# Kernel tuning notes

Hardware: AMD Instinct MI355X
Metric: run time of the kernel (lower is better)

The kernel has to match this reference:

```python
import jax, jax.numpy as jnp
import numpy as np

LATENT, H, A, L, BOS = 256, 512, 64, 128, 0


def setup_inputs() -> dict:
    key = jax.random.key(0)
    ks = jax.random.split(key, 20)
    s = 0.05
    return {
        "latent": jax.random.normal(ks[0], (4096, LATENT), jnp.float32),
        "target": jax.random.normal(ks[1], (4096, L, A), jnp.float32),
        # latent dense decoder: Linear(LATENT,H), Tanh, Linear(H,H), Tanh, Linear(H,H)
        "Wd1": jax.random.normal(ks[2], (H, LATENT), jnp.float32) * s,
        "bd1": jnp.zeros((H,), jnp.float32),
        "Wd2": jax.random.normal(ks[3], (H, H), jnp.float32) * s,
        "bd2": jnp.zeros((H,), jnp.float32),
        "Wd3": jax.random.normal(ks[4], (H, H), jnp.float32) * s,
        "bd3": jnp.zeros((H,), jnp.float32),
        # GRU (torch layout: W_ih [3H,A], W_hh [3H,H], gate order r,z,n)
        "W_ih": jax.random.normal(ks[5], (3 * H, A), jnp.float32) * s,
        "W_hh": jax.random.normal(ks[6], (3 * H, H), jnp.float32) * s,
        "b_ih": jnp.zeros((3 * H,), jnp.float32),
        "b_hh": jnp.zeros((3 * H,), jnp.float32),
        # per-step dense decoder: Linear(H,H), Tanh, Linear(H,A), Tanh, Linear(A,A)
        "Wm1": jax.random.normal(ks[7], (H, H), jnp.float32) * s,
        "bm1": jnp.zeros((H,), jnp.float32),
        "Wm2": jax.random.normal(ks[8], (A, H), jnp.float32) * s,
        "bm2": jnp.zeros((A,), jnp.float32),
        "Wm3": jax.random.normal(ks[9], (A, A), jnp.float32) * s,
        "bm3": jnp.zeros((A,), jnp.float32),
    }


def reference(latent, target, Wd1, bd1, Wd2, bd2, Wd3, bd3,
              W_ih, W_hh, b_ih, b_hh, Wm1, bm1, Wm2, bm2, Wm3, bm3):
    B = latent.shape[0]
    # initial hidden from latent: Linear-Tanh-Linear-Tanh-Linear
    h = jnp.tanh(latent @ Wd1.T + bd1)
    h = jnp.tanh(h @ Wd2.T + bd2)
    h = h @ Wd3.T + bd3  # [B, H]

    # BOS pseudo one-hot: -16 everywhere, +16 at BOS index
    bos = jnp.full((B, A), -16.0, jnp.float32).at[:, BOS].set(16.0)

    # teacher forcing: step i (1..L-1) consumes [bos, target[:,1], ..., target[:,L-2]]
    xs = jnp.concatenate([bos[None], jnp.swapaxes(target[:, 1:L - 1], 0, 1)], axis=0)  # [L-1, B, A]

    def step(h, x):
        gi = x @ W_ih.T + b_ih  # [B, 3H]
        gh = h @ W_hh.T + b_hh
        ir, iz, inn = jnp.split(gi, 3, axis=-1)
        hr, hz, hn = jnp.split(gh, 3, axis=-1)
        r = jax.nn.sigmoid(ir + hr)
        z = jax.nn.sigmoid(iz + hz)
        n = jnp.tanh(inn + r * hn)
        h_new = (1.0 - z) * n + z * h
        p = jnp.tanh(h_new @ Wm1.T + bm1)
        p = jnp.tanh(p @ Wm2.T + bm2)
        pred = p @ Wm3.T + bm3  # [B, A]
        return h_new, pred

    _, preds = jax.lax.scan(step, h, xs)  # preds: [L-1, B, A]
    y = jnp.concatenate([bos[None], preds], axis=0)  # [L, B, A]
    return jnp.swapaxes(y, 0, 1)  # [B, L, A]
```

## Files before the change

kernel.cpp:

```cpp
#include <hip/hip_runtime.h>
#include <math.h>
#include <stdint.h>

#define BATCH 4096
#define LATENT 256
#define H 512
#define A 64
#define SEQL 128
#define KCAT 576
#define CT 8
#define NSTEP 127

typedef __bf16 bf16x8 __attribute__((ext_vector_type(8)));
typedef float f32x4 __attribute__((ext_vector_type(4)));

__device__ __forceinline__ uint16_t f2bf(float f) {
    union { float f; uint32_t u; } v; v.f = f;
    uint32_t u = v.u + 0x7FFFu + ((v.u >> 16) & 1u);
    return (uint16_t)(u >> 16);
}

__device__ __forceinline__ float fast_sig(float x) {
    return __fdividef(1.0f, 1.0f + __expf(-x));
}
__device__ __forceinline__ float fast_tanh(float x) {
    return __fdividef(2.0f, 1.0f + __expf(-2.0f * x)) - 1.0f;
}

__device__ __forceinline__ f32x4 mfma16(bf16x8 a, bf16x8 b, f32x4 c) {
    return __builtin_amdgcn_mfma_f32_16x16x32_bf16(a, b, c, 0, 0, 0);
}

__device__ __forceinline__ void load_lds16(const void* g, void* l) {
    __builtin_amdgcn_global_load_lds(
        (const __attribute__((address_space(1))) uint32_t*)g,
        (__attribute__((address_space(3))) uint32_t*)l, 16, 0, 0);
}


__global__ __launch_bounds__(256) void cvt_bf16_kernel(const float* __restrict__ src,
                                                       uint16_t* __restrict__ dst, int n) {
    int idx = (blockIdx.x * 256 + threadIdx.x) * 4;
    if (idx < n) {
        float4 v = *(const float4*)(src + idx);
        dst[idx + 0] = f2bf(v.x); dst[idx + 1] = f2bf(v.y);
        dst[idx + 2] = f2bf(v.z); dst[idx + 3] = f2bf(v.w);
    }
}

__global__ __launch_bounds__(256) void wcat_kernel(const float* __restrict__ W_ih,
                                                   const float* __restrict__ W_hh,
                                                   uint16_t* __restrict__ Wcat) {
    int idx = blockIdx.x * 256 + threadIdx.x;
    if (idx < 1536 * KCAT) {
        int row = idx / KCAT, col = idx - row * KCAT;
        float v = (col < 64) ? W_ih[row * 64 + col] : W_hh[row * 512 + col - 64];
        Wcat[idx] = f2bf(v);
    }
}

__global__ __launch_bounds__(256) void bias_kernel(const float* __restrict__ b_ih,
                                                   const float* __restrict__ b_hh,
                                                   float* __restrict__ biases) {
    int idx = blockIdx.x * 256 + threadIdx.x;
    if (idx < 2048) {
        int seg = idx >> 9, j = idx & 511;
        float v;
        if (seg == 0) v = b_ih[j] + b_hh[j];
        else if (seg == 1) v = b_ih[512 + j] + b_hh[512 + j];
        else if (seg == 2) v = b_ih[1024 + j];
        else v = b_hh[1024 + j];
        biases[idx] = v;
    }
}

__global__ __launch_bounds__(256) void xall_kernel(const float* __restrict__ target,
                                                   uint16_t* __restrict__ X) {
    int idx = blockIdx.x * 256 + threadIdx.x;
    int e = idx * 4;
    int a = e & 63;
    int b = (e >> 6) & (BATCH - 1);
    int t = e >> 18;
    ushort4 o;
    if (t == 0) {
        o.x = f2bf((a == 0) ? 16.0f : -16.0f);
        uint16_t m16 = f2bf(-16.0f);
        o.y = m16; o.z = m16; o.w = m16;
    } else {
        float4 v = *(const float4*)(target + ((size_t)b * SEQL + t) * A + a);
        o.x = f2bf(v.x); o.y = f2bf(v.y); o.z = f2bf(v.z); o.w = f2bf(v.w);
    }
    *(ushort4*)(X + e) = o;
}

__global__ __launch_bounds__(256) void bosout_kernel(float* __restrict__ out) {
    int idx = blockIdx.x * 256 + threadIdx.x;
    int a = idx & (A - 1);
    int b = idx >> 6;
    out[(size_t)b * SEQL * A + a] = (a == 0) ? 16.0f : -16.0f;
}

__global__ __launch_bounds__(256)
void gemm_kernel(const uint16_t* __restrict__ Abf, int lda,
                 const uint16_t* __restrict__ Wbf,
                 const float* __restrict__ bias,
                 uint16_t* __restrict__ outb, float* __restrict__ outf,
                 int ldc, int K, int do_tanh)
{
    __shared__ __align__(16) uint16_t As[128 * 32];
    __shared__ __align__(16) uint16_t Bs[128 * 32];

    const int tid = threadIdx.x;
    const int w = tid >> 6, l = tid & 63;
    const int quad = l >> 4, lan = l & 15;
    const int m0 = blockIdx.y * 128;
    const int n0 = blockIdx.x * 128;
    const int wm = (w >> 1) * 64;
    const int wn = (w & 1) * 64;

    f32x4 acc[4][4];
#pragma unroll
    for (int i = 0; i < 4; ++i)
#pragma unroll
        for (int j = 0; j < 4; ++j) acc[i][j] = (f32x4){0.f, 0.f, 0.f, 0.f};

    const int arow = (l >> 2);
    const int kc8 = (l & 3) * 8;

    for (int k0 = 0; k0 < K; k0 += 32) {
        __syncthreads();
#pragma unroll
        for (int i = 0; i < 2; ++i) {
            int row = i * 64 + w * 16 + arow;
            load_lds16(Abf + (size_t)(m0 + row) * lda + k0 + kc8,
                       As + i * 2048 + w * 512 + l * 8);
        }
#pragma unroll
        for (int i = 0; i < 2; ++i) {
            int row = i * 64 + w * 16 + arow;
            load_lds16(Wbf + (size_t)(n0 + row) * K + k0 + kc8,
                       Bs + i * 2048 + w * 512 + l * 8);
        }
        __syncthreads();

        bf16x8 af[4], bf[4];
#pragma unroll
        for (int mi = 0; mi < 4; ++mi)
            af[mi] = *(const bf16x8*)(As + (wm + mi * 16 + lan) * 32 + quad * 8);
#pragma unroll
        for (int nj = 0; nj < 4; ++nj)
            bf[nj] = *(const bf16x8*)(Bs + (wn + nj * 16 + lan) * 32 + quad * 8);
#pragma unroll
        for (int mi = 0; mi < 4; ++mi)
#pragma unroll
            for (int nj = 0; nj < 4; ++nj)
                acc[mi][nj] = mfma16(af[mi], bf[nj], acc[mi][nj]);
    }

#pragma unroll
    for (int mi = 0; mi < 4; ++mi) {
#pragma unroll
        for (int nj = 0; nj < 4; ++nj) {
#pragma unroll
            for (int reg = 0; reg < 4; ++reg) {
                int m = m0 + wm + mi * 16 + quad * 4 + reg;
                int n = n0 + wn + nj * 16 + lan;
                float v = acc[mi][nj][reg] + bias[n];
                if (do_tanh) v = fast_tanh(v);
                if (outf) outf[(size_t)m * ldc + n] = v;
                if (outb) outb[(size_t)m * ldc + n] = f2bf(v);
            }
        }
    }
}

__global__ __launch_bounds__(256)
void gru_step_kernel(const uint16_t* __restrict__ xb,
                     const uint16_t* __restrict__ hbf,
                     const uint16_t* __restrict__ Wcat,
                     const float* __restrict__ biases,
                     const float* __restrict__ hprev,
                     float* __restrict__ hout_f,
                     uint16_t* __restrict__ hout_b)
{
    __shared__ __align__(16) uint16_t As[128 * 32];
    __shared__ __align__(16) uint16_t Bs[96 * 32];

    const int tid = threadIdx.x;
    const int w = tid >> 6, l = tid & 63;
    const int quad = l >> 4, lan = l & 15;
    const int m0 = blockIdx.y * 128;
    const int j0 = blockIdx.x * 32;
    const int wm = (w >> 1) * 64;
    const int wj = (w & 1) * 16;

    f32x4 acc[4][4];
#pragma unroll
    for (int i = 0; i < 4; ++i)
#pragma unroll
        for (int j = 0; j < 4; ++j) acc[i][j] = (f32x4){0.f, 0.f, 0.f, 0.f};

    for (int it = 0; it < KCAT / 32; ++it) {
        const int k0 = it * 32;
        const bool xseg = (k0 < 64);
        __syncthreads();
#pragma unroll
        for (int i = 0; i < 2; ++i) {
            int g = i * 256 + tid;
            int row = g >> 2, kc = (g & 3) * 8;
            const uint16_t* src = xseg
                ? (xb  + (size_t)(m0 + row) * 64  + k0 + kc)
                : (hbf + (size_t)(m0 + row) * 512 + (k0 - 64) + kc);
            load_lds16(src, As + (size_t)g * 8);
        }
        {
            int g = tid;
            int row = g >> 2, kc = (g & 3) * 8;
            int wrow = ((row >> 5) << 9) + j0 + (row & 31);
            load_lds16(Wcat + (size_t)wrow * KCAT + k0 + kc, Bs + (size_t)g * 8);
        }
        if (w < 2) {
            int g = 256 + tid;
            int row = g >> 2, kc = (g & 3) * 8;
            int wrow = ((row >> 5) << 9) + j0 + (row & 31);
            load_lds16(Wcat + (size_t)wrow * KCAT + k0 + kc, Bs + (size_t)g * 8);
        }
        __syncthreads();

        bf16x8 af[4], bfr[3];
#pragma unroll
        for (int mi = 0; mi < 4; ++mi)
            af[mi] = *(const bf16x8*)(As + (wm + mi * 16 + lan) * 32 + quad * 8);
#pragma unroll
        for (int g = 0; g < 3; ++g)
            bfr[g] = *(const bf16x8*)(Bs + (g * 32 + wj + lan) * 32 + quad * 8);

#pragma unroll
        for (int mi = 0; mi < 4; ++mi) {
            acc[mi][0] = mfma16(af[mi], bfr[0], acc[mi][0]);
            acc[mi][1] = mfma16(af[mi], bfr[1], acc[mi][1]);
        }
        if (xseg) {
#pragma unroll
            for (int mi = 0; mi < 4; ++mi)
                acc[mi][2] = mfma16(af[mi], bfr[2], acc[mi][2]);
        } else {
#pragma unroll
            for (int mi = 0; mi < 4; ++mi)
                acc[mi][3] = mfma16(af[mi], bfr[2], acc[mi][3]);
        }
    }

    const int j = j0 + wj + lan;
    const float br = biases[j], bz = biases[512 + j];
    const float bi = biases[1024 + j], bh = biases[1536 + j];
#pragma unroll
    for (int mi = 0; mi < 4; ++mi) {
#pragma unroll
        for (int reg = 0; reg < 4; ++reg) {
            int m = m0 + wm + mi * 16 + quad * 4 + reg;
            float R  = acc[mi][0][reg] + br;
            float Z  = acc[mi][1][reg] + bz;
            float I  = acc[mi][2][reg] + bi;
            float HN = acc[mi][3][reg] + bh;
            float r = fast_sig(R);
            float z = fast_sig(Z);
            float nn = fast_tanh(I + r * HN);
            float hp = hprev[(size_t)m * H + j];
            float hv = (1.0f - z) * nn + z * hp;
            hout_f[(size_t)m * H + j] = hv;
            hout_b[(size_t)m * H + j] = f2bf(hv);
        }
    }
}

__global__ __launch_bounds__(256)
void d23_kernel(const uint16_t* __restrict__ p1,
                const uint16_t* __restrict__ Wm2,
                const float* __restrict__ bm2,
                const uint16_t* __restrict__ Wm3,
                const float* __restrict__ bm3,
                float* __restrict__ out, int t0)
{
    __shared__ __align__(16) uint16_t As[128 * 32];
    __shared__ __align__(16) uint16_t B2[64 * 32];
    __shared__ __align__(16) uint16_t W3[64 * 64];
    __shared__ __align__(16) uint16_t Ps[128 * 80];

    const int tid = threadIdx.x;
    const int w = tid >> 6, l = tid & 63;
    const int quad = l >> 4, lan = l & 15;
    const int m0 = blockIdx.y * 128;
    const int wm = w * 32;

#pragma unroll
    for (int i = 0; i < 2; ++i) {
        int g = i * 256 + tid;
        int row = g >> 3, kc = (g & 7) * 8;
        load_lds16(Wm3 + (size_t)row * 64 + kc, W3 + (size_t)g * 8);
    }

    f32x4 acc[2][4];
#pragma unroll
    for (int i = 0; i < 2; ++i)
#pragma unroll
        for (int j = 0; j < 4; ++j) acc[i][j] = (f32x4){0.f, 0.f, 0.f, 0.f};

    for (int k0 = 0; k0 < 512; k0 += 32) {
        __syncthreads();
#pragma unroll
        for (int i = 0; i < 2; ++i) {
            int g = i * 256 + tid;
            int row = g >> 2, kc = (g & 3) * 8;
            load_lds16(p1 + (size_t)(m0 + row) * 512 + k0 + kc, As + (size_t)g * 8);
        }
        {
            int g = tid;
            int row = g >> 2, kc = (g & 3) * 8;
            load_lds16(Wm2 + (size_t)row * 512 + k0 + kc, B2 + (size_t)g * 8);
        }
        __syncthreads();

        bf16x8 af[2], bf[4];
#pragma unroll
        for (int mi = 0; mi < 2; ++mi)
            af[mi] = *(const bf16x8*)(As + (wm + mi * 16 + lan) * 32 + quad * 8);
#pragma unroll
        for (int nj = 0; nj < 4; ++nj)
            bf[nj] = *(const bf16x8*)(B2 + (nj * 16 + lan) * 32 + quad * 8);
#pragma unroll
        for (int mi = 0; mi < 2; ++mi)
#pragma unroll
            for (int nj = 0; nj < 4; ++nj)
                acc[mi][nj] = mfma16(af[mi], bf[nj], acc[mi][nj]);
    }

#pragma unroll
    for (int mi = 0; mi < 2; ++mi)
#pragma unroll
        for (int nj = 0; nj < 4; ++nj)
#pragma unroll
            for (int reg = 0; reg < 4; ++reg) {
                int row = wm + mi * 16 + quad * 4 + reg;
                int n = nj * 16 + lan;
                float v = fast_tanh(acc[mi][nj][reg] + bm2[n]);
                Ps[row * 80 + n] = f2bf(v);
            }
    __syncthreads();

    f32x4 a3[2][4];
#pragma unroll
    for (int i = 0; i < 2; ++i)
#pragma unroll
        for (int j = 0; j < 4; ++j) a3[i][j] = (f32x4){0.f, 0.f, 0.f, 0.f};

#pragma unroll
    for (int ks = 0; ks < 64; ks += 32) {
        bf16x8 af[2], bf[4];
#pragma unroll
        for (int mi = 0; mi < 2; ++mi)
            af[mi] = *(const bf16x8*)(Ps + (wm + mi * 16 + lan) * 80 + ks + quad * 8);
#pragma unroll
        for (int nj = 0; nj < 4; ++nj)
            bf[nj] = *(const bf16x8*)(W3 + (nj * 16 + lan) * 64 + ks + quad * 8);
#pragma unroll
        for (int mi = 0; mi < 2; ++mi)
#pragma unroll
            for (int nj = 0; nj < 4; ++nj)
                a3[mi][nj] = mfma16(af[mi], bf[nj], a3[mi][nj]);
    }

#pragma unroll
    for (int mi = 0; mi < 2; ++mi)
#pragma unroll
        for (int nj = 0; nj < 4; ++nj)
#pragma unroll
            for (int reg = 0; reg < 4; ++reg) {
                int m = m0 + wm + mi * 16 + quad * 4 + reg;
                int n = nj * 16 + lan;
                int b = m & (BATCH - 1), tl = m >> 12;
                out[(size_t)b * SEQL * A + (size_t)(t0 + tl + 1) * A + n] =
                    a3[mi][nj][reg] + bm3[n];
            }
}


extern "C" void kernel_launch(void* const* d_in, const int* in_sizes, int n_in,
                              void* d_out, int out_size, void* d_ws, size_t ws_size,
                              hipStream_t stream)
{
    const float* latent = (const float*)d_in[0];
    const float* target = (const float*)d_in[1];
    const float* Wd1 = (const float*)d_in[2];
    const float* bd1 = (const float*)d_in[3];
    const float* Wd2 = (const float*)d_in[4];
    const float* bd2 = (const float*)d_in[5];
    const float* Wd3 = (const float*)d_in[6];
    const float* bd3 = (const float*)d_in[7];
    const float* W_ih = (const float*)d_in[8];
    const float* W_hh = (const float*)d_in[9];
    const float* b_ih = (const float*)d_in[10];
    const float* b_hh = (const float*)d_in[11];
    const float* Wm1 = (const float*)d_in[12];
    const float* bm1 = (const float*)d_in[13];
    const float* Wm2 = (const float*)d_in[14];
    const float* bm2 = (const float*)d_in[15];
    const float* Wm3 = (const float*)d_in[16];
    const float* bm3 = (const float*)d_in[17];

    float* out = (float*)d_out;
    uint8_t* ws = (uint8_t*)d_ws;

    size_t off = 0;
    auto carve = [&](size_t bytes) { void* p = ws + off; off += (bytes + 255) & ~(size_t)255; return p; };
    uint16_t* latb = (uint16_t*)carve((size_t)BATCH * LATENT * 2);
    uint16_t* wd1b = (uint16_t*)carve((size_t)H * LATENT * 2);
    uint16_t* wd2b = (uint16_t*)carve((size_t)H * H * 2);
    uint16_t* wd3b = (uint16_t*)carve((size_t)H * H * 2);
    uint16_t* wm1b = (uint16_t*)carve((size_t)H * H * 2);
    uint16_t* wm2b = (uint16_t*)carve((size_t)A * H * 2);
    uint16_t* wm3b = (uint16_t*)carve((size_t)A * A * 2);
    uint16_t* wcat = (uint16_t*)carve((size_t)1536 * KCAT * 2);
    float* biases  = (float*)carve(2048 * 4);
    uint16_t* Xall = (uint16_t*)carve((size_t)NSTEP * BATCH * A * 2);
    uint16_t* t1b  = (uint16_t*)carve((size_t)BATCH * H * 2);
    uint16_t* t2b  = (uint16_t*)carve((size_t)BATCH * H * 2);
    uint16_t* h0bf = (uint16_t*)carve((size_t)BATCH * H * 2);
    float* hA      = (float*)carve((size_t)BATCH * H * 4);
    float* hB      = (float*)carve((size_t)BATCH * H * 4);
    uint16_t* hall = (uint16_t*)carve((size_t)CT * BATCH * H * 2);
    uint16_t* p1   = (uint16_t*)carve((size_t)CT * BATCH * H * 2);
    float* hbuf[2] = {hA, hB};

    dim3 blk(256);

    auto cvt = [&](const float* s, uint16_t* d, int n) {
        cvt_bf16_kernel<<<dim3((n / 4 + 255) / 256), blk, 0, stream>>>(s, d, n);
    };
    cvt(latent, latb, BATCH * LATENT);
    cvt(Wd1, wd1b, H * LATENT);
    cvt(Wd2, wd2b, H * H);
    cvt(Wd3, wd3b, H * H);
    cvt(Wm1, wm1b, H * H);
    cvt(Wm2, wm2b, A * H);
    cvt(Wm3, wm3b, A * A);
    wcat_kernel<<<dim3((1536 * KCAT + 255) / 256), blk, 0, stream>>>(W_ih, W_hh, wcat);
    bias_kernel<<<dim3(8), blk, 0, stream>>>(b_ih, b_hh, biases);
    xall_kernel<<<dim3(NSTEP * BATCH * A / 4 / 256), blk, 0, stream>>>(target, Xall);
    bosout_kernel<<<dim3(BATCH * A / 256), blk, 0, stream>>>(out);

    gemm_kernel<<<dim3(H / 128, BATCH / 128), blk, 0, stream>>>(
        latb, LATENT, wd1b, bd1, t1b, nullptr, H, LATENT, 1);
    gemm_kernel<<<dim3(H / 128, BATCH / 128), blk, 0, stream>>>(
        t1b, H, wd2b, bd2, t2b, nullptr, H, H, 1);
    gemm_kernel<<<dim3(H / 128, BATCH / 128), blk, 0, stream>>>(
        t2b, H, wd3b, bd3, h0bf, hA, H, H, 0);

    for (int c = 0; c < 16; ++c) {
        const int ct = (c == 15) ? 7 : 8;
        const int M = ct * BATCH;
        for (int tl = 0; tl < ct; ++tl) {
            const int t = c * CT + tl;
            const uint16_t* hbf = (t == 0) ? h0bf : (hall + (size_t)((t - 1) & 7) * BATCH * H);
            gru_step_kernel<<<dim3(16, 32), blk, 0, stream>>>(
                Xall + (size_t)t * BATCH * A, hbf, wcat, biases,
                hbuf[t & 1], hbuf[(t + 1) & 1], hall + (size_t)tl * BATCH * H);
        }
        gemm_kernel<<<dim3(H / 128, M / 128), blk, 0, stream>>>(
            hall, H, wm1b, bm1, p1, nullptr, H, H, 1);
        d23_kernel<<<dim3(1, M / 128), blk, 0, stream>>>(
            p1, wm2b, bm2, wm3b, bm3, out, c * CT);
    }
}
```

Measured before the change: 3.556 ms.

## Replace per-step GRU launches with persistent segment kernel using atomic step flags

Each GRU step no longer gets its own kernel launch. A persistent kernel now runs 16 timesteps per launch. Each block keeps its slice of the concatenated GRU weights resident in LDS and its fp32 hidden state in registers. Blocks sharing a batch tile wait on per-step atomic counters instead of kernel boundaries, with double-buffered and swizzled staging of the input and hidden tiles. The target-to-bf16 conversion is folded into the kernel, which removes the Xall pass. The aim is to cut launch overhead, repeated weight loads and the fp32 hidden round trips. The cost is a spin-wait sync that deadlocks unless all 256 blocks are co-resident, plus a large dynamic LDS footprint.

```diff
diff --git a/kernel.cpp b/kernel.cpp
--- a/kernel.cpp
+++ b/kernel.cpp
@@ -8,11 +8,20 @@
 #define A 64
 #define SEQL 128
 #define KCAT 576
-#define CT 8
 #define NSTEP 127
+#define SEGLEN 16
+#define NSEG 8
+
+#define MB 256
+#define JB 32
+#define BST 584
+#define AS_ELEMS (2 * 256 * 32)
+#define BS_ELEMS (96 * BST)
+#define GRU_LDS ((AS_ELEMS + BS_ELEMS) * 2)
 
 typedef __bf16 bf16x8 __attribute__((ext_vector_type(8)));
 typedef float f32x4 __attribute__((ext_vector_type(4)));
+typedef uint16_t u16x8 __attribute__((ext_vector_type(8)));
 
 __device__ __forceinline__ uint16_t f2bf(float f) {
     union { float f; uint32_t u; } v; v.f = f;
@@ -74,25 +83,6 @@
     }
 }
 
-__global__ __launch_bounds__(256) void xall_kernel(const float* __restrict__ target,
-                                                   uint16_t* __restrict__ X) {
-    int idx = blockIdx.x * 256 + threadIdx.x;
-    int e = idx * 4;
-    int a = e & 63;
-    int b = (e >> 6) & (BATCH - 1);
-    int t = e >> 18;
-    ushort4 o;
-    if (t == 0) {
-        o.x = f2bf((a == 0) ? 16.0f : -16.0f);
-        uint16_t m16 = f2bf(-16.0f);
-        o.y = m16; o.z = m16; o.w = m16;
-    } else {
-        float4 v = *(const float4*)(target + ((size_t)b * SEQL + t) * A + a);
-        o.x = f2bf(v.x); o.y = f2bf(v.y); o.z = f2bf(v.z); o.w = f2bf(v.w);
-    }
-    *(ushort4*)(X + e) = o;
-}
-
 __global__ __launch_bounds__(256) void bosout_kernel(float* __restrict__ out) {
     int idx = blockIdx.x * 256 + threadIdx.x;
     int a = idx & (A - 1);
@@ -174,104 +164,187 @@
     }
 }
 
-__global__ __launch_bounds__(256)
-void gru_step_kernel(const uint16_t* __restrict__ xb,
-                     const uint16_t* __restrict__ hbf,
-                     const uint16_t* __restrict__ Wcat,
-                     const float* __restrict__ biases,
-                     const float* __restrict__ hprev,
-                     float* __restrict__ hout_f,
-                     uint16_t* __restrict__ hout_b)
+__global__ __launch_bounds__(512)
+void gru_seg_kernel(const float* __restrict__ target,
+                    const uint16_t* __restrict__ Wcat,
+                    const float* __restrict__ biases,
+                    const uint16_t* __restrict__ hprev0,
+                    float* __restrict__ hA,
+                    uint16_t* __restrict__ hall,
+                    uint32_t* __restrict__ cnt,
+                    int t0, int nsteps)
 {
-    __shared__ __align__(16) uint16_t As[128 * 32];
-    __shared__ __align__(16) uint16_t Bs[96 * 32];
+    extern __shared__ __align__(16) uint16_t lds[];
+    uint16_t* As = lds;
+    uint16_t* Bs = lds + AS_ELEMS;
 
     const int tid = threadIdx.x;
+    const int bid = blockIdx.x;
+    const int xcd = bid & 7;
+    const int kk  = bid >> 3;
+    const int jb  = kk & 15;
+    const int mg  = xcd + ((kk >> 4) << 3);
+    const int j0  = jb * JB;
+    const int mbase = mg * MB;
+
     const int w = tid >> 6, l = tid & 63;
     const int quad = l >> 4, lan = l & 15;
-    const int m0 = blockIdx.y * 128;
-    const int j0 = blockIdx.x * 32;
     const int wm = (w >> 1) * 64;
     const int wj = (w & 1) * 16;
-
-    f32x4 acc[4][4];
-#pragma unroll
-    for (int i = 0; i < 4; ++i)
-#pragma unroll
-        for (int j = 0; j < 4; ++j) acc[i][j] = (f32x4){0.f, 0.f, 0.f, 0.f};
-
-    for (int it = 0; it < KCAT / 32; ++it) {
-        const int k0 = it * 32;
-        const bool xseg = (k0 < 64);
+    const int jcol = j0 + wj + lan;
+
+    for (int i = tid; i < 96 * 72; i += 512) {
+        int row = i / 72, c = i - row * 72;
+        int wrow = ((row >> 5) << 9) + j0 + (row & 31);
+        uint4 v = *(const uint4*)(Wcat + (size_t)wrow * KCAT + c * 8);
+        *(uint4*)(Bs + row * BST + c * 8) = v;
+    }
+
+    float hreg[4][4];
+#pragma unroll
+    for (int mi = 0; mi < 4; ++mi)
+#pragma unroll
+        for (int r = 0; r < 4; ++r)
+            hreg[mi][r] = hA[(size_t)(mbase + wm + mi * 16 + quad * 4 + r) * H + jcol];
+
+    const float br = biases[jcol], bz = biases[512 + jcol];
+    const float bi = biases[1024 + jcol], bh = biases[1536 + jcol];
+
+    const int xrow = tid >> 1;
+    const int xkh  = (tid & 1) * 16;
+    const int aswz = (lan >> 1) & 3;
+
+    auto stage_x = [&](int t, int k0, int bsel) {
+        u16x8 pk[2];
+        if (t == 0) {
+#pragma unroll
+            for (int hh = 0; hh < 2; ++hh)
+#pragma unroll
+                for (int e = 0; e < 8; ++e)
+                    pk[hh][e] = f2bf(((k0 + xkh + hh * 8 + e) == 0) ? 16.0f : -16.0f);
+        } else {
+            const float* src = target + ((size_t)(mbase + xrow) * SEQL + t) * A + k0 + xkh;
+            float4 f0 = *(const float4*)(src + 0);
+            float4 f1 = *(const float4*)(src + 4);
+            float4 f2 = *(const float4*)(src + 8);
+            float4 f3 = *(const float4*)(src + 12);
+            pk[0][0] = f2bf(f0.x); pk[0][1] = f2bf(f0.y);
+            pk[0][2] = f2bf(f0.z); pk[0][3] = f2bf(f0.w);
+            pk[0][4] = f2bf(f1.x); pk[0][5] = f2bf(f1.y);
+            pk[0][6] = f2bf(f1.z); pk[0][7] = f2bf(f1.w);
+            pk[1][0] = f2bf(f2.x); pk[1][1] = f2bf(f2.y);
+            pk[1][2] = f2bf(f2.z); pk[1][3] = f2bf(f2.w);
+            pk[1][4] = f2bf(f3.x); pk[1][5] = f2bf(f3.y);
+            pk[1][6] = f2bf(f3.z); pk[1][7] = f2bf(f3.w);
+        }
+        int swz = (xrow >> 1) & 3;
+#pragma unroll
+        for (int hh = 0; hh < 2; ++hh) {
+            int c = ((xkh >> 3) + hh) ^ swz;
+            *(u16x8*)(As + bsel * 8192 + xrow * 32 + c * 8) = pk[hh];
+        }
+    };
+
+    auto stage_h = [&](const uint16_t* hs, int k0, int bsel) {
+#pragma unroll
+        for (int i = 0; i < 2; ++i) {
+            int g = i * 512 + tid;
+            int row = g >> 2, c = g & 3;
+            int cs = c ^ ((row >> 1) & 3);
+            load_lds16(hs + (size_t)(mbase + row) * H + (k0 - 64) + cs * 8,
+                       As + bsel * 8192 + g * 8);
+        }
+    };
+
+    stage_x(t0, 0, 0);
+    __syncthreads();
+
+    for (int s = 0; s < nsteps; ++s) {
+        const int t = t0 + s;
+        const uint16_t* hs = (s == 0) ? hprev0 : (hall + (size_t)(s - 1) * BATCH * H);
+
+        f32x4 acc[4][4];
+#pragma unroll
+        for (int i = 0; i < 4; ++i)
+#pragma unroll
+            for (int j = 0; j < 4; ++j) acc[i][j] = (f32x4){0.f, 0.f, 0.f, 0.f};
+
+        for (int it = 0; it < 18; ++it) {
+            const int buf = it & 1, nb = buf ^ 1;
+            if (it == 1 && s > 0) {
+                if (tid == 0) {
+                    const uint32_t* fl = cnt + mg * SEGLEN + (s - 1);
+                    while (__hip_atomic_load(fl, __ATOMIC_ACQUIRE,
+                                             __HIP_MEMORY_SCOPE_AGENT) < 16u)
+                        __builtin_amdgcn_s_sleep(2);
+                }
+                __syncthreads();
+            }
+            if (it < 17) {
+                if (it == 0) stage_x(t, 32, nb);
+                else         stage_h(hs, (it + 1) * 32, nb);
+            } else if (s + 1 < nsteps) {
+                stage_x(t + 1, 0, nb);
+            }
+
+            const int k0 = it * 32;
+            bf16x8 af[4], bfr[3];
+#pragma unroll
+            for (int mi = 0; mi < 4; ++mi) {
+                int row = wm + mi * 16 + lan;
+                af[mi] = *(const bf16x8*)(As + buf * 8192 + row * 32 + (quad ^ aswz) * 8);
+            }
+#pragma unroll
+            for (int g = 0; g < 3; ++g)
+                bfr[g] = *(const bf16x8*)(Bs + (g * 32 + wj + lan) * BST + k0 + quad * 8);
+
+#pragma unroll
+            for (int mi = 0; mi < 4; ++mi) {
+                acc[mi][0] = mfma16(af[mi], bfr[0], acc[mi][0]);
+                acc[mi][1] = mfma16(af[mi], bfr[1], acc[mi][1]);
+            }
+            if (it < 2) {
+#pragma unroll
+                for (int mi = 0; mi < 4; ++mi)
+                    acc[mi][2] = mfma16(af[mi], bfr[2], acc[mi][2]);
+            } else {
+#pragma unroll
+                for (int mi = 0; mi < 4; ++mi)
+                    acc[mi][3] = mfma16(af[mi], bfr[2], acc[mi][3]);
+            }
+            __syncthreads();
+        }
+
+        uint16_t* ht = hall + (size_t)s * BATCH * H;
+#pragma unroll
+        for (int mi = 0; mi < 4; ++mi) {
+#pragma unroll
+            for (int r = 0; r < 4; ++r) {
+                float R  = acc[mi][0][r] + br;
+                float Z  = acc[mi][1][r] + bz;
+                float I  = acc[mi][2][r] + bi;
+                float HN = acc[mi][3][r] + bh;
+                float rg = fast_sig(R);
+                float zg = fast_sig(Z);
+                float nn = fast_tanh(I + rg * HN);
+                float hv = (1.0f - zg) * nn + zg * hreg[mi][r];
+                hreg[mi][r] = hv;
+                ht[(size_t)(mbase + wm + mi * 16 + quad * 4 + r) * H + jcol] = f2bf(hv);
+            }
+        }
         __syncthreads();
-#pragma unroll
-        for (int i = 0; i < 2; ++i) {
-            int g = i * 256 + tid;
-            int row = g >> 2, kc = (g & 3) * 8;
-            const uint16_t* src = xseg
-                ? (xb  + (size_t)(m0 + row) * 64  + k0 + kc)
-                : (hbf + (size_t)(m0 + row) * 512 + (k0 - 64) + kc);
-            load_lds16(src, As + (size_t)g * 8);
-        }
-        {
-            int g = tid;
-            int row = g >> 2, kc = (g & 3) * 8;
-            int wrow = ((row >> 5) << 9) + j0 + (row & 31);
-            load_lds16(Wcat + (size_t)wrow * KCAT + k0 + kc, Bs + (size_t)g * 8);
-        }
-        if (w < 2) {
-            int g = 256 + tid;
-            int row = g >> 2, kc = (g & 3) * 8;
-            int wrow = ((row >> 5) << 9) + j0 + (row & 31);
-            load_lds16(Wcat + (size_t)wrow * KCAT + k0 + kc, Bs + (size_t)g * 8);
-        }
-        __syncthreads();
-
-        bf16x8 af[4], bfr[3];
-#pragma unroll
-        for (int mi = 0; mi < 4; ++mi)
-            af[mi] = *(const bf16x8*)(As + (wm + mi * 16 + lan) * 32 + quad * 8);
-#pragma unroll
-        for (int g = 0; g < 3; ++g)
-            bfr[g] = *(const bf16x8*)(Bs + (g * 32 + wj + lan) * 32 + quad * 8);
-
-#pragma unroll
-        for (int mi = 0; mi < 4; ++mi) {
-            acc[mi][0] = mfma16(af[mi], bfr[0], acc[mi][0]);
-            acc[mi][1] = mfma16(af[mi], bfr[1], acc[mi][1]);
-        }
-        if (xseg) {
-#pragma unroll
-            for (int mi = 0; mi < 4; ++mi)
-                acc[mi][2] = mfma16(af[mi], bfr[2], acc[mi][2]);
-        } else {
-#pragma unroll
-            for (int mi = 0; mi < 4; ++mi)
-                acc[mi][3] = mfma16(af[mi], bfr[2], acc[mi][3]);
-        }
-    }
-
-    const int j = j0 + wj + lan;
-    const float br = biases[j], bz = biases[512 + j];
-    const float bi = biases[1024 + j], bh = biases[1536 + j];
-#pragma unroll
-    for (int mi = 0; mi < 4; ++mi) {
-#pragma unroll
-        for (int reg = 0; reg < 4; ++reg) {
-            int m = m0 + wm + mi * 16 + quad * 4 + reg;
-            float R  = acc[mi][0][reg] + br;
-            float Z  = acc[mi][1][reg] + bz;
-            float I  = acc[mi][2][reg] + bi;
-            float HN = acc[mi][3][reg] + bh;
-            float r = fast_sig(R);
-            float z = fast_sig(Z);
-            float nn = fast_tanh(I + r * HN);
-            float hp = hprev[(size_t)m * H + j];
-            float hv = (1.0f - z) * nn + z * hp;
-            hout_f[(size_t)m * H + j] = hv;
-            hout_b[(size_t)m * H + j] = f2bf(hv);
-        }
-    }
+        if (tid == 0) {
+            __threadfence();
+            (void)__hip_atomic_fetch_add(cnt + mg * SEGLEN + s, 1u,
+                                         __ATOMIC_RELEASE, __HIP_MEMORY_SCOPE_AGENT);
+        }
+    }
+
+#pragma unroll
+    for (int mi = 0; mi < 4; ++mi)
+#pragma unroll
+        for (int r = 0; r < 4; ++r)
+            hA[(size_t)(mbase + wm + mi * 16 + quad * 4 + r) * H + jcol] = hreg[mi][r];
 }
 
 __global__ __launch_bounds__(256)
@@ -422,15 +495,20 @@
     uint16_t* wm3b = (uint16_t*)carve((size_t)A * A * 2);
     uint16_t* wcat = (uint16_t*)carve((size_t)1536 * KCAT * 2);
     float* biases  = (float*)carve(2048 * 4);
-    uint16_t* Xall = (uint16_t*)carve((size_t)NSTEP * BATCH * A * 2);
     uint16_t* t1b  = (uint16_t*)carve((size_t)BATCH * H * 2);
     uint16_t* t2b  = (uint16_t*)carve((size_t)BATCH * H * 2);
     uint16_t* h0bf = (uint16_t*)carve((size_t)BATCH * H * 2);
     float* hA      = (float*)carve((size_t)BATCH * H * 4);
-    float* hB      = (float*)carve((size_t)BATCH * H * 4);
-    uint16_t* hall = (uint16_t*)carve((size_t)CT * BATCH * H * 2);
-    uint16_t* p1   = (uint16_t*)carve((size_t)CT * BATCH * H * 2);
-    float* hbuf[2] = {hA, hB};
+    uint16_t* hall = (uint16_t*)carve((size_t)SEGLEN * BATCH * H * 2);
+    uint16_t* p1   = (uint16_t*)carve((size_t)SEGLEN * BATCH * H * 2);
+    uint32_t* cnt  = (uint32_t*)carve((size_t)16 * SEGLEN * 4);
+
+    static int attr_done = 0;
+    if (!attr_done) {
+        hipFuncSetAttribute((const void*)gru_seg_kernel,
+                            hipFuncAttributeMaxDynamicSharedMemorySize, GRU_LDS);
+        attr_done = 1;
+    }
 
     dim3 blk(256);
 
@@ -446,7 +524,6 @@
     cvt(Wm3, wm3b, A * A);
     wcat_kernel<<<dim3((1536 * KCAT + 255) / 256), blk, 0, stream>>>(W_ih, W_hh, wcat);
     bias_kernel<<<dim3(8), blk, 0, stream>>>(b_ih, b_hh, biases);
-    xall_kernel<<<dim3(NSTEP * BATCH * A / 4 / 256), blk, 0, stream>>>(target, Xall);
     bosout_kernel<<<dim3(BATCH * A / 256), blk, 0, stream>>>(out);
 
     gemm_kernel<<<dim3(H / 128, BATCH / 128), blk, 0, stream>>>(
@@ -456,19 +533,17 @@
     gemm_kernel<<<dim3(H / 128, BATCH / 128), blk, 0, stream>>>(
         t2b, H, wd3b, bd3, h0bf, hA, H, H, 0);
 
-    for (int c = 0; c < 16; ++c) {
-        const int ct = (c == 15) ? 7 : 8;
-        const int M = ct * BATCH;
-        for (int tl = 0; tl < ct; ++tl) {
-            const int t = c * CT + tl;
-            const uint16_t* hbf = (t == 0) ? h0bf : (hall + (size_t)((t - 1) & 7) * BATCH * H);
-            gru_step_kernel<<<dim3(16, 32), blk, 0, stream>>>(
-                Xall + (size_t)t * BATCH * A, hbf, wcat, biases,
-                hbuf[t & 1], hbuf[(t + 1) & 1], hall + (size_t)tl * BATCH * H);
-        }
+    for (int seg = 0; seg < NSEG; ++seg) {
+        const int t0 = seg * SEGLEN;
+        const int ns = (seg == NSEG - 1) ? (NSTEP - t0) : SEGLEN;
+        hipMemsetAsync(cnt, 0, (size_t)16 * SEGLEN * 4, stream);
+        const uint16_t* hp0 = (seg == 0) ? h0bf : hall + (size_t)(SEGLEN - 1) * BATCH * H;
+        gru_seg_kernel<<<dim3(256), dim3(512), GRU_LDS, stream>>>(
+            target, wcat, biases, hp0, hA, hall, cnt, t0, ns);
+        const int M = ns * BATCH;
         gemm_kernel<<<dim3(H / 128, M / 128), blk, 0, stream>>>(
             hall, H, wm1b, bm1, p1, nullptr, H, H, 1);
         d23_kernel<<<dim3(1, M / 128), blk, 0, stream>>>(
-            p1, wm2b, bm2, wm3b, bm3, out, c * CT);
-    }
-}
+            p1, wm2b, bm2, wm3b, bm3, out, t0);
+    }
+}
```

New measurement: 4.619 ms. 29.9% more time.
